# Performance work log

Measured on AMD Instinct MI355X. Metric: run time of the kernel, lower is better.

## Reference

```python
import jax, jax.numpy as jnp
import numpy as np

N = 100000      # nodes
E = 1600000     # edges (avg degree 16)
F_IN = 512      # input node features
H = 8           # heads in conv1
D = 8           # per-head dim in conv1
C = 7           # classes
NEG_SLOPE = 0.2 # PyG GATConv default leaky_relu slope


def setup_inputs() -> dict:
    key = jax.random.key(0)
    ks = jax.random.split(key, 10)
    s = 0.05
    return {
        "x": jax.random.normal(ks[0], (N, F_IN), jnp.float32),
        "edge_index": jax.random.randint(ks[1], (2, E), 0, N, dtype=jnp.int64),
        "W1": jax.random.normal(ks[2], (F_IN, H * D), jnp.float32) * s,
        "a1_src": jax.random.normal(ks[3], (H, D), jnp.float32) * s,
        "a1_dst": jax.random.normal(ks[4], (H, D), jnp.float32) * s,
        "b1": jnp.zeros((H * D,), jnp.float32),
        "W2": jax.random.normal(ks[5], (H * D, C), jnp.float32) * s,
        "a2_src": jax.random.normal(ks[6], (1, C), jnp.float32) * s,
        "a2_dst": jax.random.normal(ks[7], (1, C), jnp.float32) * s,
        "b2": jnp.zeros((C,), jnp.float32),
    }


def _gat_conv(x, src, dst, W, a_src, a_dst, b, heads, dim, concat, n):
    # linear transform -> [N, H, D]
    h = (x @ W).reshape(n, heads, dim)
    # per-node attention halves: [N, H]
    al_src = jnp.einsum('nhd,hd->nh', h, a_src)
    al_dst = jnp.einsum('nhd,hd->nh', h, a_dst)
    # per-edge logits, leaky relu: [E', H]
    e = jax.nn.leaky_relu(al_src[src] + al_dst[dst], NEG_SLOPE)
    # segment softmax over incoming edges of each dst node
    m = jax.lax.stop_gradient(jax.ops.segment_max(e, dst, num_segments=n))
    p = jnp.exp(e - m[dst])
    z = jax.ops.segment_sum(p, dst, num_segments=n)
    alpha = p / z[dst]                                   # [E', H]
    # weighted scatter-add of source messages -> [N, H, D]
    out = jax.ops.segment_sum(h[src] * alpha[..., None], dst, num_segments=n)
    out = out.reshape(n, heads * dim) if concat else out.mean(axis=1)
    return out + b


def reference(x, edge_index, W1, a1_src, a1_dst, b1, W2, a2_src, a2_dst, b2):
    n = x.shape[0]
    # PyG GATConv default: add self loops
    loops = jnp.arange(n, dtype=edge_index.dtype)
    src = jnp.concatenate([edge_index[0], loops])
    dst = jnp.concatenate([edge_index[1], loops])
    h = _gat_conv(x, src, dst, W1, a1_src, a1_dst, b1, H, D, True, n)
    h = jax.nn.elu(h)
    out = _gat_conv(h, src, dst, W2, a2_src, a2_dst, b2, 1, C, False, n)
    return jax.nn.log_softmax(out, axis=1)
```

## Files before the change

### kernel.cpp

```cpp
#include <hip/hip_runtime.h>
#include <math.h>

#define N_NODES 100000
#define N_EDGES 1600000
#define F_IN 512
#define HD 64
#define CC 7
#define NKT (F_IN / 32)
#define BS 64
#define NBK ((N_NODES + BS - 1) / BS)
#define ECAP 2048
#define SCHUNK 4096
#define SBLK ((N_EDGES + SCHUNK - 1) / SCHUNK)
#define GEMMBLKS ((N_NODES + 63) / 64)
#define W1WORK (NKT * 4 * 64)

typedef __attribute__((ext_vector_type(8))) short short8;
typedef __attribute__((ext_vector_type(4))) float f32x4;

__device__ inline unsigned short f2bf(float f) {
    union { float f; unsigned u; } v; v.f = f;
    unsigned u = v.u;
    return (unsigned short)((u + 0x7fffu + ((u >> 16) & 1u)) >> 16);
}
__device__ inline float bf2f(unsigned short b) {
    union { unsigned u; float f; } v; v.u = ((unsigned)b) << 16;
    return v.f;
}

__global__ __launch_bounds__(256) void prep_kernel(const float* __restrict__ W1,
                                                   unsigned short* __restrict__ wf,
                                                   int* __restrict__ bcur) {
    if (blockIdx.x == 16) {
        for (int i = threadIdx.x; i < NBK; i += 256) bcur[i] = 0;
        return;
    }
    int t = blockIdx.x * 256 + threadIdx.x;
    if (t >= W1WORK) return;
    int lane = t & 63;
    int ct = (t >> 6) & 3;
    int kt = t >> 8;
    int k0 = kt * 32 + (lane >> 4) * 8;
    int col = ct * 16 + (lane & 15);
    unsigned short* dst = wf + (size_t)t * 8;
    #pragma unroll
    for (int j = 0; j < 8; ++j) dst[j] = f2bf(W1[(k0 + j) * HD + col]);
}

__global__ __launch_bounds__(256) void fused_kernel(
        const int* __restrict__ ei, int* __restrict__ bcur, int* __restrict__ pairs,
        const float* __restrict__ x, const unsigned short* __restrict__ wf,
        const float* __restrict__ a1s, const float* __restrict__ a1d,
        unsigned short* __restrict__ h1b, float* __restrict__ als,
        float* __restrict__ ald) {
    __shared__ float ls[64 * 65];
    const int bid = blockIdx.x;
    const int tid = threadIdx.x;
    if (bid % 5 == 0) {
        const int sb = bid / 5;
        int* cnt = (int*)ls;
        int* bas = cnt + NBK;
        const int e0 = sb * SCHUNK;
        int e1 = e0 + SCHUNK; if (e1 > N_EDGES) e1 = N_EDGES;
        for (int b = tid; b < NBK; b += 256) cnt[b] = 0;
        __syncthreads();
        for (int i = e0 + tid; i < e1; i += 256)
            atomicAdd(&cnt[ei[N_EDGES + i] >> 6], 1);
        __syncthreads();
        const int boff = (sb * 263) % NBK;
        for (int bb = tid; bb < NBK; bb += 256) {
            int b = bb + boff; if (b >= NBK) b -= NBK;
            int c = cnt[b];
            bas[b] = c ? atomicAdd(&bcur[b], c) : 0;
            cnt[b] = 0;
        }
        __syncthreads();
        for (int i = e0 + tid; i < e1; i += 256) {
            int s = ei[i];
            int t = ei[N_EDGES + i];
            int b = t >> 6;
            int pos = bas[b] + atomicAdd(&cnt[b], 1);
            if (pos < ECAP) pairs[(size_t)b * ECAP + pos] = (s << 6) | (t & (BS - 1));
        }
        return;
    }
    const int gb = bid - bid / 5 - 1;
    const int wave = tid >> 6;
    const int lane = tid & 63;
    int arow = gb * 64 + wave * 16 + (lane & 15);
    if (arow >= N_NODES) arow = N_NODES - 1;
    const float* xp = x + (size_t)arow * F_IN + (lane >> 4) * 8;
    const short8* wp = (const short8*)wf;

    f32x4 acc[4] = {};
    #pragma unroll 4
    for (int kt = 0; kt < NKT; ++kt) {
        f32x4 a0 = *(const f32x4*)(xp + kt * 32);
        f32x4 a1 = *(const f32x4*)(xp + kt * 32 + 4);
        union { short8 s; unsigned short u[8]; } af;
        af.u[0] = f2bf(a0.x); af.u[1] = f2bf(a0.y);
        af.u[2] = f2bf(a0.z); af.u[3] = f2bf(a0.w);
        af.u[4] = f2bf(a1.x); af.u[5] = f2bf(a1.y);
        af.u[6] = f2bf(a1.z); af.u[7] = f2bf(a1.w);
        #pragma unroll
        for (int ct = 0; ct < 4; ++ct) {
            short8 bf = wp[kt * 256 + ct * 64 + lane];
            acc[ct] = __builtin_amdgcn_mfma_f32_16x16x32_bf16(af.s, bf, acc[ct], 0, 0, 0);
        }
    }
    const int lrow_base = wave * 16 + (lane >> 4) * 4;
    const int ocol = lane & 15;
    #pragma unroll
    for (int ct = 0; ct < 4; ++ct) {
        #pragma unroll
        for (int r = 0; r < 4; ++r) {
            int lrow = lrow_base + r;
            int orow = gb * 64 + lrow;
            ls[lrow * 65 + ct * 16 + ocol] = acc[ct][r];
            if (orow < N_NODES)
                h1b[(size_t)orow * HD + ct * 16 + ocol] = f2bf(acc[ct][r]);
        }
    }
    __syncthreads();
    #pragma unroll
    for (int task = tid; task < 64 * 8; task += 256) {
        int r = task >> 3, h = task & 7;
        int node = gb * 64 + r;
        if (node < N_NODES) {
            float s = 0.f, d = 0.f;
            #pragma unroll
            for (int k = 0; k < 8; ++k) {
                float v = ls[r * 65 + h * 8 + k];
                s += v * a1s[h * 8 + k];
                d += v * a1d[h * 8 + k];
            }
            als[node * 8 + h] = s;
            ald[node * 8 + h] = d;
        }
    }
}

__global__ __launch_bounds__(256) void sortcsr_kernel(const int* __restrict__ bcur,
                                                      const int* __restrict__ pairs,
                                                      int* __restrict__ csr_src,
                                                      int* __restrict__ rowptr,
                                                      int* __restrict__ rowcnt) {
    __shared__ int cnt[BS];
    __shared__ int start[BS];
    __shared__ int srcl[ECAP];
    const int tid = threadIdx.x;
    const int lane = tid & 63;
    const int n0 = blockIdx.x * BS;
    const size_t bbase = (size_t)blockIdx.x * ECAP;
    const int* bp = pairs + bbase;
    int ne = bcur[blockIdx.x]; if (ne > ECAP) ne = ECAP;
    if (tid < BS) cnt[tid] = 0;
    __syncthreads();
    for (int k = tid; k < ne; k += 256)
        atomicAdd(&cnt[bp[k] & (BS - 1)], 1);
    __syncthreads();
    if (tid < 64) {
        int a = cnt[lane];
        int xx = a;
        #pragma unroll
        for (int o = 1; o < 64; o <<= 1) { int u = __shfl_up(xx, o, 64); if (lane >= o) xx += u; }
        start[lane] = xx - a;
        cnt[lane] = 0;
    }
    __syncthreads();
    for (int k = tid; k < ne; k += 256) {
        int v = bp[k];
        int ln = v & (BS - 1);
        int pos = start[ln] + atomicAdd(&cnt[ln], 1);
        srcl[pos] = v >> 6;
    }
    __syncthreads();
    for (int k = tid; k < ne; k += 256) csr_src[bbase + k] = srcl[k];
    if (tid < BS) {
        int node = n0 + tid;
        if (node < N_NODES) {
            rowptr[node] = (int)bbase + start[tid];
            rowcnt[node] = cnt[tid];
        }
    }
}

__global__ __launch_bounds__(256) void gather1_kernel(
        const int* __restrict__ rowptr, const int* __restrict__ rowcnt,
        const int* __restrict__ csr_src,
        const float* __restrict__ als, const float* __restrict__ ald,
        const unsigned short* __restrict__ h1b, const float* __restrict__ b1,
        const float* __restrict__ W2, const float* __restrict__ a2s,
        const float* __restrict__ a2d,
        unsigned short* __restrict__ g2b, float* __restrict__ al2s,
        float* __restrict__ al2d) {
    int node = (blockIdx.x * 256 + threadIdx.x) >> 6;
    if (node >= N_NODES) return;
    const int lane = threadIdx.x & 63;
    const int h = lane >> 3;
    const int e8 = lane & 7, base8 = lane & 56;
    const int rs = rowptr[node], ncnt = rowcnt[node];
    const float aldt = ald[node * 8 + h];
    float e = als[node * 8 + h] + aldt;
    e = (e >= 0.f) ? e : 0.2f * e;
    float p = __expf(e);
    float acc = p * bf2f(h1b[(size_t)node * HD + lane]);
    float z = p;
    int k = 0;
    for (; k + 8 <= ncnt; k += 8) {
        int s_own = csr_src[rs + k + e8];
        int se[8];
        #pragma unroll
        for (int q = 0; q < 8; ++q) se[q] = __shfl(s_own, base8 | q, 64);
        float ve[8];
        #pragma unroll
        for (int q = 0; q < 8; ++q) ve[q] = bf2f(h1b[(size_t)se[q] * HD + lane]);
        float ee = als[s_own * 8 + h] + aldt;
        ee = (ee >= 0.f) ? ee : 0.2f * ee;
        float pv = __expf(ee);
        #pragma unroll
        for (int q = 0; q < 8; ++q) {
            float pe = __shfl(pv, base8 | q, 64);
            z += pe;
            acc = fmaf(pe, ve[q], acc);
        }
    }
    if (k < ncnt) {
        const int m = ncnt - k;
        int idx = rs + k + ((e8 < m) ? e8 : (m - 1));
        int s_own = csr_src[idx];
        int se[8];
        #pragma unroll
        for (int q = 0; q < 8; ++q) se[q] = __shfl(s_own, base8 | q, 64);
        float ee = als[s_own * 8 + h] + aldt;
        ee = (ee >= 0.f) ? ee : 0.2f * ee;
        float pv = __expf(ee);
        for (int q = 0; q < m; ++q) {
            float pe = __shfl(pv, base8 | q, 64);
            float ve = bf2f(h1b[(size_t)se[q] * HD + lane]);
            z += pe;
            acc = fmaf(pe, ve, acc);
        }
    }
    float v = acc / z + b1[lane];
    v = (v > 0.f) ? v : (__expf(v) - 1.f);
    float w[CC];
    #pragma unroll
    for (int c = 0; c < CC; ++c) w[c] = W2[lane * CC + c];
    float g[CC];
    #pragma unroll
    for (int c = 0; c < CC; ++c) {
        float r = v * w[c];
        #pragma unroll
        for (int d = 1; d < 64; d <<= 1) r += __shfl_xor(r, d, 64);
        g[c] = r;
    }
    float s2 = 0.f, d2 = 0.f;
    #pragma unroll
    for (int c = 0; c < CC; ++c) { s2 += g[c] * a2s[c]; d2 += g[c] * a2d[c]; }
    if (lane < CC) g2b[(size_t)node * 8 + lane] = f2bf(g[lane]);
    if (lane == CC) g2b[(size_t)node * 8 + CC] = 0;
    if (lane == 8) al2s[node] = s2;
    if (lane == 9) al2d[node] = d2;
}

__global__ __launch_bounds__(256) void gather2_kernel(
        const int* __restrict__ rowptr, const int* __restrict__ rowcnt,
        const int* __restrict__ csr_src,
        const float* __restrict__ al2s, const float* __restrict__ al2d,
        const unsigned short* __restrict__ g2b, const float* __restrict__ b2,
        float* __restrict__ out) {
    int gid = blockIdx.x * 256 + threadIdx.x;
    int n = gid >> 3, c = gid & 7;
    if (n >= N_NODES) return;
    const int lane = threadIdx.x & 63;
    const int base8 = lane & 56;
    const int rs = rowptr[n], ncnt = rowcnt[n];
    const float adn = al2d[n];
    float e = al2s[n] + adn;
    e = (e >= 0.f) ? e : 0.2f * e;
    float p = __expf(e);
    float acc = p * bf2f(g2b[(size_t)n * 8 + c]);
    float z = p;
    int k = 0;
    for (; k + 8 <= ncnt; k += 8) {
        int s_own = csr_src[rs + k + c];
        int se[8];
        #pragma unroll
        for (int q = 0; q < 8; ++q) se[q] = __shfl(s_own, base8 | q, 64);
        float ve[8];
        #pragma unroll
        for (int q = 0; q < 8; ++q) ve[q] = bf2f(g2b[(size_t)se[q] * 8 + c]);
        float ee = al2s[s_own] + adn;
        ee = (ee >= 0.f) ? ee : 0.2f * ee;
        float pv = __expf(ee);
        #pragma unroll
        for (int q = 0; q < 8; ++q) {
            float pe = __shfl(pv, base8 | q, 64);
            z += pe;
            acc = fmaf(pe, ve[q], acc);
        }
    }
    if (k < ncnt) {
        const int m = ncnt - k;
        int idx = rs + k + ((c < m) ? c : (m - 1));
        int s_own = csr_src[idx];
        int se[8];
        #pragma unroll
        for (int q = 0; q < 8; ++q) se[q] = __shfl(s_own, base8 | q, 64);
        float ee = al2s[s_own] + adn;
        ee = (ee >= 0.f) ? ee : 0.2f * ee;
        float pv = __expf(ee);
        for (int q = 0; q < m; ++q) {
            float pe = __shfl(pv, base8 | q, 64);
            float ve = bf2f(g2b[(size_t)se[q] * 8 + c]);
            z += pe;
            acc = fmaf(pe, ve, acc);
        }
    }
    float o = (c < CC) ? (acc / z + b2[c]) : -1e30f;
    float m2 = o;
    #pragma unroll
    for (int d = 1; d < 8; d <<= 1) m2 = fmaxf(m2, __shfl_xor(m2, d, 8));
    float ex = (c < CC) ? __expf(o - m2) : 0.f;
    float sum = ex;
    #pragma unroll
    for (int d = 1; d < 8; d <<= 1) sum += __shfl_xor(sum, d, 8);
    float lse = m2 + __logf(sum);
    if (c < CC) out[(size_t)n * CC + c] = o - lse;
}

extern "C" void kernel_launch(void* const* d_in, const int* in_sizes, int n_in,
                              void* d_out, int out_size, void* d_ws, size_t ws_size,
                              hipStream_t stream) {
    const float* x   = (const float*)d_in[0];
    const int*   ei  = (const int*)d_in[1];
    const float* W1  = (const float*)d_in[2];
    const float* a1s = (const float*)d_in[3];
    const float* a1d = (const float*)d_in[4];
    const float* b1  = (const float*)d_in[5];
    const float* W2  = (const float*)d_in[6];
    const float* a2s = (const float*)d_in[7];
    const float* a2d = (const float*)d_in[8];
    const float* b2  = (const float*)d_in[9];
    float* out = (float*)d_out;

    char* base = (char*)d_ws;
    size_t off = 0;
    auto alloc = [&](size_t bytes) { char* p = base + off; off = (off + bytes + 63) & ~(size_t)63; return p; };
    unsigned short* h1b = (unsigned short*)alloc((size_t)N_NODES * HD * 2);
    unsigned short* wf  = (unsigned short*)alloc((size_t)W1WORK * 8 * 2);
    float* als  = (float*)alloc((size_t)N_NODES * 8 * 4);
    float* ald  = (float*)alloc((size_t)N_NODES * 8 * 4);
    unsigned short* g2b = (unsigned short*)alloc((size_t)N_NODES * 8 * 2);
    float* al2s = (float*)alloc((size_t)N_NODES * 4);
    float* al2d = (float*)alloc((size_t)N_NODES * 4);
    int* bcur   = (int*)alloc((size_t)NBK * 4);
    int* rowptr = (int*)alloc((size_t)N_NODES * 4);
    int* rowcnt = (int*)alloc((size_t)N_NODES * 4);
    int* csr_src= (int*)alloc((size_t)NBK * ECAP * 4);
    int* pairs  = (int*)alloc((size_t)NBK * ECAP * 4);

    prep_kernel<<<17, 256, 0, stream>>>(W1, wf, bcur);
    fused_kernel<<<SBLK + GEMMBLKS, 256, 0, stream>>>(
        ei, bcur, pairs, x, wf, a1s, a1d, h1b, als, ald);
    sortcsr_kernel<<<NBK, 256, 0, stream>>>(bcur, pairs, csr_src, rowptr, rowcnt);
    gather1_kernel<<<(N_NODES * 64 + 255) / 256, 256, 0, stream>>>(
        rowptr, rowcnt, csr_src, als, ald, h1b, b1, W2, a2s, a2d, g2b, al2s, al2d);
    gather2_kernel<<<(N_NODES * 8 + 255) / 256, 256, 0, stream>>>(
        rowptr, rowcnt, csr_src, al2s, al2d, g2b, b2, out);
}
```

Before: 196.5 us.

## Replace global atomic bucket cursors with per-chunk count/offset matrices for edge binning

Each edge-chunk block now locally counting-sorts its edges by destination bucket in shared memory. It writes the sorted chunk contiguously, along with per-chunk bucket counts (M) and exclusive offsets (S). This replaces the global atomicAdd on the bucket cursors and the scattered pair writes. The CSR kernel then reads its column of M and S, prefix-sums the counts, and gathers its bucket's segments from every chunk. The intent is to remove global atomics and make the pair writes coalesced. The costs are extra M/S traffic, strided column reads in sortcsr, and larger shared memory in the fused kernel, which may lower GEMM-block occupancy.

```diff
diff --git a/kernel.cpp b/kernel.cpp
--- a/kernel.cpp
+++ b/kernel.cpp
@@ -14,6 +14,7 @@
 #define SBLK ((N_EDGES + SCHUNK - 1) / SCHUNK)
 #define GEMMBLKS ((N_NODES + 63) / 64)
 #define W1WORK (NKT * 4 * 64)
+#define SHMI (2 * NBK + SCHUNK)
 
 typedef __attribute__((ext_vector_type(8))) short short8;
 typedef __attribute__((ext_vector_type(4))) float f32x4;
@@ -29,12 +30,7 @@
 }
 
 __global__ __launch_bounds__(256) void prep_kernel(const float* __restrict__ W1,
-                                                   unsigned short* __restrict__ wf,
-                                                   int* __restrict__ bcur) {
-    if (blockIdx.x == 16) {
-        for (int i = threadIdx.x; i < NBK; i += 256) bcur[i] = 0;
-        return;
-    }
+                                                   unsigned short* __restrict__ wf) {
     int t = blockIdx.x * 256 + threadIdx.x;
     if (t >= W1WORK) return;
     int lane = t & 63;
@@ -48,30 +44,67 @@
 }
 
 __global__ __launch_bounds__(256) void fused_kernel(
-        const int* __restrict__ ei, int* __restrict__ bcur, int* __restrict__ pairs,
+        const int* __restrict__ ei, int* __restrict__ pairs,
+        int* __restrict__ M, int* __restrict__ S,
         const float* __restrict__ x, const unsigned short* __restrict__ wf,
         const float* __restrict__ a1s, const float* __restrict__ a1d,
         unsigned short* __restrict__ h1b, float* __restrict__ als,
         float* __restrict__ ald) {
-    __shared__ float ls[64 * 65];
+    __shared__ int shm[SHMI];
     const int bid = blockIdx.x;
     const int tid = threadIdx.x;
     if (bid % 5 == 0) {
+        int* cnt   = shm;
+        int* start = shm + NBK;
+        int* stage = shm + 2 * NBK;
         const int sb = bid / 5;
-        int* cnt = (int*)ls;
-        int* bas = cnt + NBK;
         const int e0 = sb * SCHUNK;
         int e1 = e0 + SCHUNK; if (e1 > N_EDGES) e1 = N_EDGES;
+        const int nloc = e1 - e0;
+        const int wave = tid >> 6, lane = tid & 63;
         for (int b = tid; b < NBK; b += 256) cnt[b] = 0;
         __syncthreads();
         for (int i = e0 + tid; i < e1; i += 256)
             atomicAdd(&cnt[ei[N_EDGES + i] >> 6], 1);
         __syncthreads();
-        const int boff = (sb * 263) % NBK;
-        for (int bb = tid; bb < NBK; bb += 256) {
-            int b = bb + boff; if (b >= NBK) b -= NBK;
-            int c = cnt[b];
-            bas[b] = c ? atomicAdd(&bcur[b], c) : 0;
+        for (int b = tid; b < NBK; b += 256) M[(size_t)sb * NBK + b] = cnt[b];
+        {
+            const int wbeg = wave * 400;
+            int wend = wbeg + 400; if (wend > NBK) wend = NBK;
+            int carry = 0;
+            for (int base = wbeg; base < wend; base += 64) {
+                int idx = base + lane;
+                int v = (idx < wend) ? cnt[idx] : 0;
+                int xx = v;
+                #pragma unroll
+                for (int o = 1; o < 64; o <<= 1) {
+                    int u = __shfl_up(xx, o, 64);
+                    if (lane >= o) xx += u;
+                }
+                if (idx < wend) start[idx] = carry + xx - v;
+                carry += __shfl(xx, 63, 64);
+            }
+            if (lane == 0) stage[wave] = carry;
+        }
+        __syncthreads();
+        if (tid == 0) {
+            int o = 0;
+            #pragma unroll
+            for (int w = 0; w < 4; ++w) { int v = stage[w]; stage[w] = o; o += v; }
+        }
+        __syncthreads();
+        {
+            const int woff = stage[wave];
+            const int wbeg = wave * 400;
+            int wend = wbeg + 400; if (wend > NBK) wend = NBK;
+            for (int base = wbeg; base < wend; base += 64) {
+                int idx = base + lane;
+                if (idx < wend) start[idx] += woff;
+            }
+        }
+        __syncthreads();
+        for (int b = tid; b < NBK; b += 256) {
+            S[(size_t)sb * NBK + b] = start[b];
             cnt[b] = 0;
         }
         __syncthreads();
@@ -79,11 +112,14 @@
             int s = ei[i];
             int t = ei[N_EDGES + i];
             int b = t >> 6;
-            int pos = bas[b] + atomicAdd(&cnt[b], 1);
-            if (pos < ECAP) pairs[(size_t)b * ECAP + pos] = (s << 6) | (t & (BS - 1));
-        }
+            int pos = start[b] + atomicAdd(&cnt[b], 1);
+            stage[pos] = (s << 6) | (t & (BS - 1));
+        }
+        __syncthreads();
+        for (int k = tid; k < nloc; k += 256) pairs[(size_t)sb * SCHUNK + k] = stage[k];
         return;
     }
+    float* ls = (float*)shm;
     const int gb = bid - bid / 5 - 1;
     const int wave = tid >> 6;
     const int lane = tid & 63;
@@ -140,24 +176,59 @@
     }
 }
 
-__global__ __launch_bounds__(256) void sortcsr_kernel(const int* __restrict__ bcur,
+__global__ __launch_bounds__(256) void sortcsr_kernel(const int* __restrict__ M,
+                                                      const int* __restrict__ S,
                                                       const int* __restrict__ pairs,
                                                       int* __restrict__ csr_src,
                                                       int* __restrict__ rowptr,
                                                       int* __restrict__ rowcnt) {
+    __shared__ int mcol[SBLK];
+    __shared__ int scol[SBLK];
+    __shared__ int pcol[SBLK + 1];
+    __shared__ int stage[ECAP];
+    __shared__ int srcl[ECAP];
     __shared__ int cnt[BS];
     __shared__ int start[BS];
-    __shared__ int srcl[ECAP];
     const int tid = threadIdx.x;
     const int lane = tid & 63;
-    const int n0 = blockIdx.x * BS;
-    const size_t bbase = (size_t)blockIdx.x * ECAP;
-    const int* bp = pairs + bbase;
-    int ne = bcur[blockIdx.x]; if (ne > ECAP) ne = ECAP;
+    const int b = blockIdx.x;
+    const int n0 = b * BS;
+    const size_t bbase = (size_t)b * ECAP;
+    for (int j = tid; j < SBLK; j += 256) {
+        mcol[j] = M[(size_t)j * NBK + b];
+        scol[j] = S[(size_t)j * NBK + b];
+    }
     if (tid < BS) cnt[tid] = 0;
     __syncthreads();
+    if (tid < 64) {
+        int carry = 0;
+        for (int base = 0; base < SBLK; base += 64) {
+            int idx = base + lane;
+            int v = (idx < SBLK) ? mcol[idx] : 0;
+            int xx = v;
+            #pragma unroll
+            for (int o = 1; o < 64; o <<= 1) {
+                int u = __shfl_up(xx, o, 64);
+                if (lane >= o) xx += u;
+            }
+            if (idx < SBLK) pcol[idx] = carry + xx - v;
+            carry += __shfl(xx, 63, 64);
+        }
+        if (lane == 0) pcol[SBLK] = carry;
+    }
+    __syncthreads();
+    int ne = pcol[SBLK]; if (ne > ECAP) ne = ECAP;
+    for (int j = tid; j < SBLK; j += 256) {
+        int len = mcol[j], dst = pcol[j];
+        const int* src = pairs + (size_t)j * SCHUNK + scol[j];
+        for (int q = 0; q < len; ++q) {
+            int d = dst + q;
+            if (d < ECAP) stage[d] = src[q];
+        }
+    }
+    __syncthreads();
     for (int k = tid; k < ne; k += 256)
-        atomicAdd(&cnt[bp[k] & (BS - 1)], 1);
+        atomicAdd(&cnt[stage[k] & (BS - 1)], 1);
     __syncthreads();
     if (tid < 64) {
         int a = cnt[lane];
@@ -169,7 +240,7 @@
     }
     __syncthreads();
     for (int k = tid; k < ne; k += 256) {
-        int v = bp[k];
+        int v = stage[k];
         int ln = v & (BS - 1);
         int pos = start[ln] + atomicAdd(&cnt[ln], 1);
         srcl[pos] = v >> 6;
@@ -355,16 +426,17 @@
     unsigned short* g2b = (unsigned short*)alloc((size_t)N_NODES * 8 * 2);
     float* al2s = (float*)alloc((size_t)N_NODES * 4);
     float* al2d = (float*)alloc((size_t)N_NODES * 4);
-    int* bcur   = (int*)alloc((size_t)NBK * 4);
+    int* M      = (int*)alloc((size_t)SBLK * NBK * 4);
+    int* S      = (int*)alloc((size_t)SBLK * NBK * 4);
     int* rowptr = (int*)alloc((size_t)N_NODES * 4);
     int* rowcnt = (int*)alloc((size_t)N_NODES * 4);
     int* csr_src= (int*)alloc((size_t)NBK * ECAP * 4);
-    int* pairs  = (int*)alloc((size_t)NBK * ECAP * 4);
-
-    prep_kernel<<<17, 256, 0, stream>>>(W1, wf, bcur);
+    int* pairs  = (int*)alloc((size_t)SBLK * SCHUNK * 4);
+
+    prep_kernel<<<16, 256, 0, stream>>>(W1, wf);
     fused_kernel<<<SBLK + GEMMBLKS, 256, 0, stream>>>(
-        ei, bcur, pairs, x, wf, a1s, a1d, h1b, als, ald);
-    sortcsr_kernel<<<NBK, 256, 0, stream>>>(bcur, pairs, csr_src, rowptr, rowcnt);
+        ei, pairs, M, S, x, wf, a1s, a1d, h1b, als, ald);
+    sortcsr_kernel<<<NBK, 256, 0, stream>>>(M, S, pairs, csr_src, rowptr, rowcnt);
     gather1_kernel<<<(N_NODES * 64 + 255) / 256, 256, 0, stream>>>(
         rowptr, rowcnt, csr_src, als, ald, h1b, b1, W2, a2s, a2d, g2b, al2s, al2d);
     gather2_kernel<<<(N_NODES * 8 + 255) / 256, 256, 0, stream>>>(
```

After: 217.1 us. 1.1x slower.
